# Optimization experiments

Hardware: AMD Instinct MI355X
Metric: run time of the kernel (lower is better)

The kernel has to match this reference:

```python
import jax, jax.numpy as jnp
import numpy as np

N, F_IN, F_OUT, K = 4096, 32, 32, 2
NEG_SLOPE = 0.2
MASK_VAL = -9e15


def _sparse_mat(kv, km, density=0.01):
    vals = jax.random.normal(kv, (N, N), dtype=jnp.float32)
    mask = jax.random.uniform(km, (N, N)) < density
    return vals * mask


def setup_inputs() -> dict:
    key = jax.random.key(0)
    ks = jax.random.split(key, 12)
    x = jax.random.normal(ks[0], (N, F_IN), dtype=jnp.float32)
    Ld = _sparse_mat(ks[1], ks[2])
    Lu = _sparse_mat(ks[3], ks[4])
    P = jax.random.normal(ks[5], (N, N), dtype=jnp.float32) / np.sqrt(N)
    W1 = jax.random.normal(ks[6], (K, F_IN, F_OUT), dtype=jnp.float32) * 0.1
    W2 = jax.random.normal(ks[7], (K, F_IN, F_OUT), dtype=jnp.float32) * 0.1
    W0 = jax.random.normal(ks[8], (F_IN, F_OUT), dtype=jnp.float32) * 0.1
    att1 = jax.random.normal(ks[9], (2 * F_OUT * K, 1), dtype=jnp.float32) * 0.1
    att2 = jax.random.normal(ks[10], (2 * F_OUT * K, 1), dtype=jnp.float32) * 0.1
    return {"x": x, "Ld": Ld, "Lu": Lu, "P": P, "W1": W1, "W2": W2,
            "W0": W0, "att1": att1, "att2": att2}


def _branch(x, L, W, att):
    # W: [K, F_in, F_out]; precompute x @ W[k] for all k -> [K, N, F_out]
    Kk, _, Fo = W.shape
    xw = jnp.einsum('nf,kfo->kno', x, W)
    # torch.cat([x@W[k]], dim=1) == transpose+reshape of xw
    xcat = jnp.transpose(xw, (1, 0, 2)).reshape(x.shape[0], Kk * Fo)
    d = Fo * Kk
    e = xcat @ att[:d] + (xcat @ att[d:]).T            # [N, N]
    e = jax.nn.leaky_relu(e, negative_slope=NEG_SLOPE)
    e = jnp.where(L != 0, e, MASK_VAL)
    alpha = jax.nn.softmax(e, axis=1)                   # row softmax, no dropout (eval)
    z = alpha @ xw[0]
    a = alpha
    for k in range(1, Kk):
        a = a @ L
        z = z + a @ xw[k]
    return z


def reference(x, Ld, Lu, P, W1, W2, W0, att1, att2):
    z1 = _branch(x, Ld, W1, att1)
    z2 = _branch(x, Lu, W2, att2)
    x0 = P @ (x @ W0)
    return z1 + z2 + x0
```

## Files before the change

kernel.cpp:

```cpp
#include <hip/hip_runtime.h>
#include <hip/hip_bf16.h>

#define NN 4096
#define CAP 128
#define KS 8

typedef __attribute__((ext_vector_type(8))) short bf16x8;
typedef __attribute__((ext_vector_type(4))) float f32x4;

__device__ __forceinline__ float lrelu(float v) { return v >= 0.f ? v : 0.2f * v; }

__device__ __forceinline__ ushort f2bu(float f) {
    unsigned u = __float_as_uint(f);
    return (ushort)((u + 0x7FFFu + ((u >> 16) & 1u)) >> 16);
}

__global__ __launch_bounds__(256) void k_prep(
    const float* __restrict__ x,
    const float* __restrict__ W1, const float* __restrict__ W2,
    const float* __restrict__ W0,
    const float* __restrict__ att1, const float* __restrict__ att2,
    float* __restrict__ xwA1, float* __restrict__ xwB1,
    float* __restrict__ xwA2, float* __restrict__ xwB2,
    float* __restrict__ a1, float* __restrict__ b1,
    float* __restrict__ a2, float* __restrict__ b2,
    __hip_bfloat16* __restrict__ Bt)
{
    __shared__ float wl[5120];
    __shared__ float xs[256];
    const int t = threadIdx.x;
    for (int i = t; i < 2048; i += 256) { wl[i] = W1[i]; wl[2048 + i] = W2[i]; }
    for (int i = t; i < 1024; i += 256) wl[4096 + i] = W0[i];
    const int rowBase = blockIdx.x * 8;
    xs[t] = x[rowBase * 32 + t];
    __syncthreads();

    const int o = t & 31, r = t >> 5;
    const int row = rowBase + r;
    const float* xr = &xs[r * 32];
    float vA1 = 0.f, vB1 = 0.f, vA2 = 0.f, vB2 = 0.f, v0 = 0.f;
#pragma unroll
    for (int f = 0; f < 32; ++f) {
        const float xv = xr[f];
        vA1 += xv * wl[f * 32 + o];
        vB1 += xv * wl[1024 + f * 32 + o];
        vA2 += xv * wl[2048 + f * 32 + o];
        vB2 += xv * wl[3072 + f * 32 + o];
        v0  += xv * wl[4096 + f * 32 + o];
    }
    xwA1[row * 32 + o] = vA1;
    xwB1[row * 32 + o] = vB1;
    xwA2[row * 32 + o] = vA2;
    xwB2[row * 32 + o] = vB2;
    ((ushort*)Bt)[(size_t)o * NN + row] = f2bu(v0);

    float pa1 = vA1 * att1[o]      + vB1 * att1[32 + o];
    float pb1 = vA1 * att1[64 + o] + vB1 * att1[96 + o];
    float pa2 = vA2 * att2[o]      + vB2 * att2[32 + o];
    float pb2 = vA2 * att2[64 + o] + vB2 * att2[96 + o];
#pragma unroll
    for (int m = 1; m <= 16; m <<= 1) {
        pa1 += __shfl_xor(pa1, m); pb1 += __shfl_xor(pb1, m);
        pa2 += __shfl_xor(pa2, m); pb2 += __shfl_xor(pb2, m);
    }
    if (o == 0) { a1[row] = pa1; b1[row] = pb1; a2[row] = pa2; b2[row] = pb2; }
}

__global__ __launch_bounds__(256) void k_scan(
    const float* __restrict__ Ld, const float* __restrict__ Lu,
    const float* __restrict__ xwB1, const float* __restrict__ xwB2,
    const float* __restrict__ xwA1, const float* __restrict__ xwA2,
    int* __restrict__ csr, int* __restrict__ cntArr,
    float* __restrict__ u1, float* __restrict__ u2)
{
    const int w = threadIdx.x >> 6, lane = threadIdx.x & 63;
    const int row = blockIdx.x * 4 + w;
    const int br  = blockIdx.y;
    const float* L   = br ? Lu : Ld;
    const float* xwB = br ? xwB2 : xwB1;
    const float* xwA = br ? xwA2 : xwA1;
    int*   csrB = csr + (size_t)br * NN * CAP;
    int*   cntB = cntArr + br * NN;
    float* u    = br ? u2 : u1;

    __shared__ int2 sle[4][CAP];
    int2* se = sle[w];

    const float4* L4 = (const float4*)(L + (size_t)row * NN);
    const unsigned long long lt = (1ull << lane) - 1ull;

    float4 buf[8];
#pragma unroll
    for (int it = 0; it < 8; ++it) buf[it] = L4[it * 64 + lane];
    int runbase = 0;
#pragma unroll
    for (int it = 0; it < 16; ++it) {
        const float4 vv = buf[it & 7];
        if (it < 8) buf[it & 7] = L4[(it + 8) * 64 + lane];
        const unsigned long long m0 = __ballot(vv.x != 0.f);
        const unsigned long long m1 = __ballot(vv.y != 0.f);
        const unsigned long long m2 = __ballot(vv.z != 0.f);
        const unsigned long long m3 = __ballot(vv.w != 0.f);
        const int p0 = __popcll(m0), p1 = __popcll(m1), p2 = __popcll(m2);
        const int c0 = (it * 64 + lane) * 4;
        int s;
        s = runbase + __popcll(m0 & lt);
        if (vv.x != 0.f && s < CAP) { int2 e; e.x = c0;     e.y = __float_as_int(vv.x); se[s] = e; }
        s = runbase + p0 + __popcll(m1 & lt);
        if (vv.y != 0.f && s < CAP) { int2 e; e.x = c0 + 1; e.y = __float_as_int(vv.y); se[s] = e; }
        s = runbase + p0 + p1 + __popcll(m2 & lt);
        if (vv.z != 0.f && s < CAP) { int2 e; e.x = c0 + 2; e.y = __float_as_int(vv.z); se[s] = e; }
        s = runbase + p0 + p1 + p2 + __popcll(m3 & lt);
        if (vv.w != 0.f && s < CAP) { int2 e; e.x = c0 + 3; e.y = __float_as_int(vv.w); se[s] = e; }
        runbase += p0 + p1 + p2 + __popcll(m3);
    }
    const int cnt  = min(runbase, CAP);
    const int cp16 = min((cnt + 15) & ~15, CAP);
    {
        const int s = cnt + lane;
        if (s < cp16) { int2 e; e.x = 0; e.y = 0; se[s] = e; }
    }

    if (lane < cp16)      csrB[(size_t)row * CAP + lane]      = se[lane].x;
    if (lane + 64 < cp16) csrB[(size_t)row * CAP + lane + 64] = se[lane + 64].x;
    if (lane == 0) cntB[row] = cnt;

    const int o = lane & 31, g = lane >> 5;
    float acc = 0.f;
    const int nb = cp16 >> 3;
    for (int j = 0; j < nb; ++j) {
        float wv[4], xv[4];
#pragma unroll
        for (int q = 0; q < 4; ++q) {
            const int2 e = se[8 * j + 2 * q + g];
            wv[q] = __int_as_float(e.y);
            xv[q] = xwB[(size_t)e.x * 32 + o];
        }
#pragma unroll
        for (int q = 0; q < 4; ++q) acc += wv[q] * xv[q];
    }
    acc += __shfl_xor(acc, 32);
    if (lane < 32) u[(size_t)row * 32 + o] = acc + xwA[(size_t)row * 32 + o];
}

__global__ __launch_bounds__(256) void k_attn(
    const int* __restrict__ csr, const int* __restrict__ cntArr,
    const float* __restrict__ a1, const float* __restrict__ b1,
    const float* __restrict__ a2, const float* __restrict__ b2,
    const float* __restrict__ u1, const float* __restrict__ u2,
    float* __restrict__ z1, float* __restrict__ z2)
{
    const int br = blockIdx.y;
    const int* csrB = csr + (size_t)br * NN * CAP;
    const int* cntB = cntArr + br * NN;
    const float* aA = br ? a2 : a1;
    const float* bA = br ? b2 : b1;
    const float* U  = br ? u2 : u1;
    float* z = br ? z2 : z1;

    __shared__ float sw[4 * CAP];
    __shared__ int   sci[4 * CAP];
    const int w = threadIdx.x >> 6, lane = threadIdx.x & 63;
    const int row = blockIdx.x * 4 + w;
    const int cnt = cntB[row];
    const int cp16 = min((cnt + 15) & ~15, CAP);
    const float ai = aA[row];
    const int* ci = csrB + (size_t)row * CAP;
    float* swg = sw + w * CAP;
    int*   scg = sci + w * CAP;

    int id0 = 0, id1 = 0;
    if (lane < cp16)      id0 = ci[lane];
    if (lane + 64 < cp16) id1 = ci[lane + 64];
    float e0 = (lane < cnt)      ? lrelu(ai + bA[id0]) : -1e30f;
    float e1 = (lane + 64 < cnt) ? lrelu(ai + bA[id1]) : -1e30f;
    float lmax = fmaxf(e0, e1);
#pragma unroll
    for (int m = 1; m <= 32; m <<= 1) lmax = fmaxf(lmax, __shfl_xor(lmax, m));
    const float w0 = __expf(e0 - lmax), w1 = __expf(e1 - lmax);
    float ssum = w0 + w1;
#pragma unroll
    for (int m = 1; m <= 32; m <<= 1) ssum += __shfl_xor(ssum, m);
    swg[lane] = w0; swg[lane + 64] = w1;
    scg[lane] = id0; scg[lane + 64] = id1;

    const int o = lane & 31, h = lane >> 5;
    float acc = 0.f;
    const int nb = cp16 >> 3;
    if (cnt > 0) {
        float wgA[4], uvA[4];
#pragma unroll
        for (int q = 0; q < 4; ++q) {
            const int s = h + 2 * q;
            wgA[q] = swg[s];
            uvA[q] = U[(size_t)scg[s] * 32 + o];
        }
        for (int j = 1; j < nb; ++j) {
            float wgB[4], uvB[4];
#pragma unroll
            for (int q = 0; q < 4; ++q) {
                const int s = h + 8 * j + 2 * q;
                wgB[q] = swg[s];
                uvB[q] = U[(size_t)scg[s] * 32 + o];
            }
#pragma unroll
            for (int q = 0; q < 4; ++q) acc += wgA[q] * uvA[q];
#pragma unroll
            for (int q = 0; q < 4; ++q) { wgA[q] = wgB[q]; uvA[q] = uvB[q]; }
        }
#pragma unroll
        for (int q = 0; q < 4; ++q) acc += wgA[q] * uvA[q];
    }
    acc += __shfl_xor(acc, 32);
    if (lane < 32) z[(size_t)row * 32 + o] = (cnt > 0) ? acc / ssum : 0.f;
}

__global__ __launch_bounds__(256) void k_pgemm(
    const float* __restrict__ P, const ushort* __restrict__ Bt,
    float* __restrict__ partial)
{
    __shared__ ushort sA[2][16 * 64 * 8];
    __shared__ ushort sB[2][8 * 64 * 8];
    const int t = threadIdx.x;
    const int row0 = blockIdx.x * 64;
    const int ks = blockIdx.y;
    const float4*  P4  = (const float4*)P;
    const ushort4* Bt4 = (const ushort4*)Bt;

    const int lane = t & 63, w = t >> 6;

    f32x4 acc0 = {0.f, 0.f, 0.f, 0.f};
    f32x4 acc1 = {0.f, 0.f, 0.f, 0.f};

    auto stageA = [&](int c, int buf) {
        const int kc4 = (ks * 512 + c * 128) >> 2;
#pragma unroll
        for (int j = 0; j < 8; ++j) {
            const int i = t + 256 * j;
            const int row = i >> 5, q = i & 31;
            const float4 v = P4[(size_t)(row0 + row) * 1024 + kc4 + q];
            ushort4 u;
            u.x = f2bu(v.x); u.y = f2bu(v.y); u.z = f2bu(v.z); u.w = f2bu(v.w);
            const int wi = row >> 4, m = row & 15;
            const int kk = q >> 3, quad = (q >> 1) & 3, jj = q & 1;
            *(ushort4*)&sA[buf][(((wi * 4 + kk) * 64) + quad * 16 + m) * 8 + jj * 4] = u;
        }
    };
    auto stageB = [&](int c, int buf) {
        const int kc4 = (ks * 512 + c * 128) >> 2;
#pragma unroll
        for (int j = 0; j < 4; ++j) {
            const int i = t + 256 * j;
            const int o = i >> 5, q = i & 31;
            const ushort4 u = Bt4[(size_t)o * 1024 + kc4 + q];
            const int nt = o >> 4, n = o & 15;
            const int kk = q >> 3, quad = (q >> 1) & 3, jj = q & 1;
            *(ushort4*)&sB[buf][(((kk * 2 + nt) * 64) + quad * 16 + n) * 8 + jj * 4] = u;
        }
    };
    auto compute = [&](int buf) {
        const ushort* pa = &sA[buf][(w * 4) * 64 * 8 + lane * 8];
        const ushort* pb = &sB[buf][lane * 8];
#pragma unroll
        for (int kk = 0; kk < 4; ++kk) {
            const bf16x8 a  = *(const bf16x8*)(pa + kk * 512);
            const bf16x8 b0 = *(const bf16x8*)(pb + kk * 1024);
            const bf16x8 b1 = *(const bf16x8*)(pb + kk * 1024 + 512);
            acc0 = __builtin_amdgcn_mfma_f32_16x16x32_bf16(a, b0, acc0, 0, 0, 0);
            acc1 = __builtin_amdgcn_mfma_f32_16x16x32_bf16(a, b1, acc1, 0, 0, 0);
        }
    };

    stageA(0, 0); stageB(0, 0);
    __syncthreads();
    for (int c = 0; c < 4; ++c) {
        if (c < 3) { stageA(c + 1, (c + 1) & 1); stageB(c + 1, (c + 1) & 1); }
        compute(c & 1);
        __syncthreads();
    }

    const int m = lane & 15, quad = lane >> 4;
    float* out = partial + ((size_t)ks * NN + row0 + w * 16 + quad * 4) * 32;
#pragma unroll
    for (int r = 0; r < 4; ++r) {
        out[r * 32 + m]      = acc0[r];
        out[r * 32 + 16 + m] = acc1[r];
    }
}

__global__ __launch_bounds__(256) void k_combine(
    const float4* __restrict__ z1, const float4* __restrict__ z2,
    const float4* __restrict__ partial, float4* __restrict__ out)
{
    const int i = blockIdx.x * 256 + threadIdx.x;
    const float4 a = z1[i], b = z2[i];
    float rx = a.x + b.x, ry = a.y + b.y, rz = a.z + b.z, rw = a.w + b.w;
#pragma unroll
    for (int p = 0; p < KS; ++p) {
        const float4 c = partial[p * 32768 + i];
        rx += c.x; ry += c.y; rz += c.z; rw += c.w;
    }
    float4 rr; rr.x = rx; rr.y = ry; rr.z = rz; rr.w = rw;
    out[i] = rr;
}

extern "C" void kernel_launch(void* const* d_in, const int* in_sizes, int n_in,
                              void* d_out, int out_size, void* d_ws, size_t ws_size,
                              hipStream_t stream) {
    (void)in_sizes; (void)n_in; (void)out_size; (void)ws_size;
    const float* x    = (const float*)d_in[0];
    const float* Ld   = (const float*)d_in[1];
    const float* Lu   = (const float*)d_in[2];
    const float* P    = (const float*)d_in[3];
    const float* W1   = (const float*)d_in[4];
    const float* W2   = (const float*)d_in[5];
    const float* W0   = (const float*)d_in[6];
    const float* att1 = (const float*)d_in[7];
    const float* att2 = (const float*)d_in[8];

    float* ws = (float*)d_ws;
    float* xwA1 = ws;
    float* xwB1 = ws + 131072;
    float* xwA2 = ws + 262144;
    float* xwB2 = ws + 393216;
    float* u1   = ws + 524288;
    float* u2   = ws + 655360;
    float* z1   = ws + 786432;
    float* z2   = ws + 917504;
    float* a1   = ws + 1048576;
    float* b1   = ws + 1052672;
    float* a2   = ws + 1056768;
    float* b2   = ws + 1060864;
    float* partial = ws + 1064960;
    __hip_bfloat16* Bt = (__hip_bfloat16*)(ws + 1064960 + KS * 131072);
    int* csr = (int*)(ws + 1064960 + KS * 131072 + 65536);
    int* cnt = (int*)(ws + 1064960 + KS * 131072 + 65536 + 1048576);

    k_prep<<<512, 256, 0, stream>>>(x, W1, W2, W0, att1, att2,
                                    xwA1, xwB1, xwA2, xwB2, a1, b1, a2, b2, Bt);
    k_scan<<<dim3(NN / 4, 2), 256, 0, stream>>>(Ld, Lu, xwB1, xwB2, xwA1, xwA2,
                                                csr, cnt, u1, u2);
    k_attn<<<dim3(NN / 4, 2), 256, 0, stream>>>(csr, cnt, a1, b1, a2, b2,
                                                u1, u2, z1, z2);
    k_pgemm<<<dim3(64, KS), 256, 0, stream>>>(P, (const ushort*)Bt, partial);
    k_combine<<<128, 256, 0, stream>>>((const float4*)z1, (const float4*)z2,
                                       (const float4*)partial, (float4*)d_out);
}
```

Measured before the change: 230.6 us.

## Split dense-mask scan into block-per-row CSR build and separate gather kernel

Replaces the wave-per-row scan of Ld/Lu, which also did the xwB gather, with a k_csr kernel that has one 256-thread block per row. It handles both branches, uses a shared-memory prefix over wave counts, and writes (col, val) pairs straight to global memory. A new k_gather kernel reads that CSR to compute u, and k_attn reads the int2 entries. The aim is more memory-level parallelism when streaming the 2x64MB dense matrices, at the cost of an extra kernel launch and an extra global round-trip for the CSR values.

```diff
diff --git a/kernel.cpp b/kernel.cpp
--- a/kernel.cpp
+++ b/kernel.cpp
@@ -66,64 +66,97 @@
     if (o == 0) { a1[row] = pa1; b1[row] = pb1; a2[row] = pa2; b2[row] = pb2; }
 }
 
-__global__ __launch_bounds__(256) void k_scan(
+__global__ __launch_bounds__(256) void k_csr(
     const float* __restrict__ Ld, const float* __restrict__ Lu,
+    int2* __restrict__ csrv, int* __restrict__ cntArr)
+{
+    const int row = blockIdx.x;
+    const int t = threadIdx.x, lane = t & 63, w = t >> 6;
+    __shared__ int wcnt[16];
+
+    float4 v[8];
+    const float4* A4 = (const float4*)(Ld + (size_t)row * NN);
+    const float4* B4 = (const float4*)(Lu + (size_t)row * NN);
+#pragma unroll
+    for (int it = 0; it < 4; ++it) { v[it] = A4[it * 256 + t]; v[4 + it] = B4[it * 256 + t]; }
+
+    const unsigned long long lt = (1ull << lane) - 1ull;
+#pragma unroll
+    for (int br = 0; br < 2; ++br) {
+        int2* out = csrv + ((size_t)br * NN + row) * CAP;
+        int tots[4];
+#pragma unroll
+        for (int it = 0; it < 4; ++it) {
+            const float4 fv = v[br * 4 + it];
+            tots[it] = __popcll(__ballot(fv.x != 0.f)) + __popcll(__ballot(fv.y != 0.f))
+                     + __popcll(__ballot(fv.z != 0.f)) + __popcll(__ballot(fv.w != 0.f));
+        }
+        __syncthreads();
+        if (lane == 0) {
+            int4 tv; tv.x = tots[0]; tv.y = tots[1]; tv.z = tots[2]; tv.w = tots[3];
+            *(int4*)&wcnt[w * 4] = tv;
+        }
+        __syncthreads();
+        const int4 ca = *(const int4*)&wcnt[0];
+        const int4 cb = *(const int4*)&wcnt[4];
+        const int4 cc = *(const int4*)&wcnt[8];
+        const int4 cd = *(const int4*)&wcnt[12];
+        const int cs[16] = {ca.x, ca.y, ca.z, ca.w, cb.x, cb.y, cb.z, cb.w,
+                            cc.x, cc.y, cc.z, cc.w, cd.x, cd.y, cd.z, cd.w};
+        int total = 0;
+#pragma unroll
+        for (int k2 = 0; k2 < 16; ++k2) total += cs[k2];
+        int base = 0;
+#pragma unroll
+        for (int k2 = 0; k2 < 16; ++k2) base += (k2 < (w << 2)) ? cs[k2] : 0;
+        const int cnt  = min(total, CAP);
+        const int cp16 = min((cnt + 15) & ~15, CAP);
+
+#pragma unroll
+        for (int it = 0; it < 4; ++it) {
+            const float4 fv = v[br * 4 + it];
+            const unsigned long long m0 = __ballot(fv.x != 0.f);
+            const unsigned long long m1 = __ballot(fv.y != 0.f);
+            const unsigned long long m2 = __ballot(fv.z != 0.f);
+            const unsigned long long m3 = __ballot(fv.w != 0.f);
+            const int p0 = __popcll(m0), p1 = __popcll(m1), p2 = __popcll(m2);
+            const int c0 = (it * 256 + t) * 4;
+            int s;
+            s = base + __popcll(m0 & lt);
+            if (fv.x != 0.f && s < CAP) { int2 e; e.x = c0;     e.y = __float_as_int(fv.x); out[s] = e; }
+            s = base + p0 + __popcll(m1 & lt);
+            if (fv.y != 0.f && s < CAP) { int2 e; e.x = c0 + 1; e.y = __float_as_int(fv.y); out[s] = e; }
+            s = base + p0 + p1 + __popcll(m2 & lt);
+            if (fv.z != 0.f && s < CAP) { int2 e; e.x = c0 + 2; e.y = __float_as_int(fv.z); out[s] = e; }
+            s = base + p0 + p1 + p2 + __popcll(m3 & lt);
+            if (fv.w != 0.f && s < CAP) { int2 e; e.x = c0 + 3; e.y = __float_as_int(fv.w); out[s] = e; }
+            base += p0 + p1 + p2 + __popcll(m3);
+        }
+        if (t >= cnt && t < cp16) { int2 e; e.x = 0; e.y = 0; out[t] = e; }
+        if (t == 0) cntArr[br * NN + row] = cnt;
+    }
+}
+
+__global__ __launch_bounds__(256) void k_gather(
+    const int2* __restrict__ csrv, const int* __restrict__ cntArr,
     const float* __restrict__ xwB1, const float* __restrict__ xwB2,
     const float* __restrict__ xwA1, const float* __restrict__ xwA2,
-    int* __restrict__ csr, int* __restrict__ cntArr,
     float* __restrict__ u1, float* __restrict__ u2)
 {
+    __shared__ int2 sle[4][CAP];
     const int w = threadIdx.x >> 6, lane = threadIdx.x & 63;
     const int row = blockIdx.x * 4 + w;
     const int br  = blockIdx.y;
-    const float* L   = br ? Lu : Ld;
     const float* xwB = br ? xwB2 : xwB1;
     const float* xwA = br ? xwA2 : xwA1;
-    int*   csrB = csr + (size_t)br * NN * CAP;
-    int*   cntB = cntArr + br * NN;
-    float* u    = br ? u2 : u1;
-
-    __shared__ int2 sle[4][CAP];
+    float* u = br ? u2 : u1;
+
+    const int cnt  = cntArr[br * NN + row];
+    const int cp16 = min((cnt + 15) & ~15, CAP);
+    const int2* ci = csrv + ((size_t)br * NN + row) * CAP;
     int2* se = sle[w];
-
-    const float4* L4 = (const float4*)(L + (size_t)row * NN);
-    const unsigned long long lt = (1ull << lane) - 1ull;
-
-    float4 buf[8];
-#pragma unroll
-    for (int it = 0; it < 8; ++it) buf[it] = L4[it * 64 + lane];
-    int runbase = 0;
-#pragma unroll
-    for (int it = 0; it < 16; ++it) {
-        const float4 vv = buf[it & 7];
-        if (it < 8) buf[it & 7] = L4[(it + 8) * 64 + lane];
-        const unsigned long long m0 = __ballot(vv.x != 0.f);
-        const unsigned long long m1 = __ballot(vv.y != 0.f);
-        const unsigned long long m2 = __ballot(vv.z != 0.f);
-        const unsigned long long m3 = __ballot(vv.w != 0.f);
-        const int p0 = __popcll(m0), p1 = __popcll(m1), p2 = __popcll(m2);
-        const int c0 = (it * 64 + lane) * 4;
-        int s;
-        s = runbase + __popcll(m0 & lt);
-        if (vv.x != 0.f && s < CAP) { int2 e; e.x = c0;     e.y = __float_as_int(vv.x); se[s] = e; }
-        s = runbase + p0 + __popcll(m1 & lt);
-        if (vv.y != 0.f && s < CAP) { int2 e; e.x = c0 + 1; e.y = __float_as_int(vv.y); se[s] = e; }
-        s = runbase + p0 + p1 + __popcll(m2 & lt);
-        if (vv.z != 0.f && s < CAP) { int2 e; e.x = c0 + 2; e.y = __float_as_int(vv.z); se[s] = e; }
-        s = runbase + p0 + p1 + p2 + __popcll(m3 & lt);
-        if (vv.w != 0.f && s < CAP) { int2 e; e.x = c0 + 3; e.y = __float_as_int(vv.w); se[s] = e; }
-        runbase += p0 + p1 + p2 + __popcll(m3);
-    }
-    const int cnt  = min(runbase, CAP);
-    const int cp16 = min((cnt + 15) & ~15, CAP);
-    {
-        const int s = cnt + lane;
-        if (s < cp16) { int2 e; e.x = 0; e.y = 0; se[s] = e; }
-    }
-
-    if (lane < cp16)      csrB[(size_t)row * CAP + lane]      = se[lane].x;
-    if (lane + 64 < cp16) csrB[(size_t)row * CAP + lane + 64] = se[lane + 64].x;
-    if (lane == 0) cntB[row] = cnt;
+    if (lane < cp16)      se[lane]      = ci[lane];
+    if (lane + 64 < cp16) se[lane + 64] = ci[lane + 64];
 
     const int o = lane & 31, g = lane >> 5;
     float acc = 0.f;
@@ -144,14 +177,13 @@
 }
 
 __global__ __launch_bounds__(256) void k_attn(
-    const int* __restrict__ csr, const int* __restrict__ cntArr,
+    const int2* __restrict__ csrv, const int* __restrict__ cntArr,
     const float* __restrict__ a1, const float* __restrict__ b1,
     const float* __restrict__ a2, const float* __restrict__ b2,
     const float* __restrict__ u1, const float* __restrict__ u2,
     float* __restrict__ z1, float* __restrict__ z2)
 {
     const int br = blockIdx.y;
-    const int* csrB = csr + (size_t)br * NN * CAP;
     const int* cntB = cntArr + br * NN;
     const float* aA = br ? a2 : a1;
     const float* bA = br ? b2 : b1;
@@ -165,13 +197,13 @@
     const int cnt = cntB[row];
     const int cp16 = min((cnt + 15) & ~15, CAP);
     const float ai = aA[row];
-    const int* ci = csrB + (size_t)row * CAP;
+    const int2* ci = csrv + ((size_t)br * NN + row) * CAP;
     float* swg = sw + w * CAP;
     int*   scg = sci + w * CAP;
 
     int id0 = 0, id1 = 0;
-    if (lane < cp16)      id0 = ci[lane];
-    if (lane + 64 < cp16) id1 = ci[lane + 64];
+    if (lane < cp16)      id0 = ci[lane].x;
+    if (lane + 64 < cp16) id1 = ci[lane + 64].x;
     float e0 = (lane < cnt)      ? lrelu(ai + bA[id0]) : -1e30f;
     float e1 = (lane + 64 < cnt) ? lrelu(ai + bA[id1]) : -1e30f;
     float lmax = fmaxf(e0, e1);
@@ -332,15 +364,16 @@
     float* a2   = ws + 1056768;
     float* b2   = ws + 1060864;
     float* partial = ws + 1064960;
-    __hip_bfloat16* Bt = (__hip_bfloat16*)(ws + 1064960 + KS * 131072);
-    int* csr = (int*)(ws + 1064960 + KS * 131072 + 65536);
-    int* cnt = (int*)(ws + 1064960 + KS * 131072 + 65536 + 1048576);
+    __hip_bfloat16* Bt = (__hip_bfloat16*)(ws + 2113536);
+    int2* csrv = (int2*)(ws + 2179072);
+    int*  cnt  = (int*)(ws + 4276224);
 
     k_prep<<<512, 256, 0, stream>>>(x, W1, W2, W0, att1, att2,
                                     xwA1, xwB1, xwA2, xwB2, a1, b1, a2, b2, Bt);
-    k_scan<<<dim3(NN / 4, 2), 256, 0, stream>>>(Ld, Lu, xwB1, xwB2, xwA1, xwA2,
-                                                csr, cnt, u1, u2);
-    k_attn<<<dim3(NN / 4, 2), 256, 0, stream>>>(csr, cnt, a1, b1, a2, b2,
+    k_csr<<<NN, 256, 0, stream>>>(Ld, Lu, csrv, cnt);
+    k_gather<<<dim3(NN / 4, 2), 256, 0, stream>>>(csrv, cnt, xwB1, xwB2,
+                                                  xwA1, xwA2, u1, u2);
+    k_attn<<<dim3(NN / 4, 2), 256, 0, stream>>>(csrv, cnt, a1, b1, a2, b2,
                                                 u1, u2, z1, z2);
     k_pgemm<<<dim3(64, KS), 256, 0, stream>>>(P, (const ushort*)Bt, partial);
     k_combine<<<128, 256, 0, stream>>>((const float4*)z1, (const float4*)z2,
```

After: 235.9 us. 1.02x slower.
